# Performance work log

Measured on AMD Instinct MI355X. Metric: run time of the kernel, lower is better.

## Reference

```python
import jax, jax.numpy as jnp
import numpy as np
import math

B, N, IN_DIM, HID, OUT = 16, 1024, 3, 32, 4
RATIO = 0.2
K1 = math.ceil(RATIO * N)    # 205 nodes kept after pool 1
K2 = math.ceil(RATIO * K1)   # 41 nodes kept after pool 2
AVG_DEG = 16.0
BN_EPS = 1e-5


def setup_inputs() -> dict:
    key = jax.random.key(0)
    ks = jax.random.split(key, 16)
    x = jax.random.normal(ks[0], (B, N, IN_DIM), jnp.float32)
    # sparse random undirected adjacency (binary edge weights = 1), no self loops
    u = jax.random.uniform(ks[1], (B, N, N))
    A = (u < (AVG_DEG / N)).astype(jnp.float32)
    A = jnp.maximum(A, jnp.swapaxes(A, -1, -2))
    A = A * (1.0 - jnp.eye(N, dtype=jnp.float32))
    g = lambda i, shp: (jax.random.normal(ks[i], shp, jnp.float32) * 0.1)
    params = dict(
        Wd0=g(2, (IN_DIM, HID)), bd0=jnp.zeros((HID,), jnp.float32),
        Wd1=g(3, (HID, HID)),    bd1=jnp.zeros((HID,), jnp.float32),
        Wd2=g(4, (HID, HID)),    bd2=jnp.zeros((HID,), jnp.float32),
        Wu0=g(5, (HID, HID)),    bu0=jnp.zeros((HID,), jnp.float32),
        Wu1=g(6, (HID, HID)),    bu1=jnp.zeros((HID,), jnp.float32),
        p1=g(7, (HID,)), p2=g(8, (HID,)),
        gamma=jnp.ones((HID,), jnp.float32), beta=jnp.zeros((HID,), jnp.float32),
        W1=g(9, (HID, HID)),  b1=jnp.zeros((HID,), jnp.float32),
        W2=g(10, (HID, HID)), b2=jnp.zeros((HID,), jnp.float32),
        W3=g(11, (HID, OUT)), b3=jnp.zeros((OUT,), jnp.float32),
    )
    return {"x": x, "adj": A, **params}


def _gcn(A, x, W, b):
    # GCNConv(improved=True): A_hat = A + 2I, symmetric normalization
    n = A.shape[-1]
    A_hat = A + 2.0 * jnp.eye(n, dtype=A.dtype)
    deg = A_hat.sum(-1)                              # [B, n]
    dis = jnp.where(deg > 0, jax.lax.rsqrt(deg), 0.0)
    A_norm = dis[..., :, None] * A_hat * dis[..., None, :]
    return jnp.einsum('bij,bjf->bif', A_norm, x @ W) + b


def _augment(A):
    # GraphUNet.augment_adj: add self loops (w=1), square adjacency, drop diag
    n = A.shape[-1]
    eye = jnp.eye(n, dtype=A.dtype)
    Bm = A + eye
    A2 = jnp.einsum('bij,bjk->bik', Bm, Bm)
    return A2 * (1.0 - eye)


def _topk_pool(A, x, p, k):
    # TopKPooling: score = tanh(x.p / ||p||), keep top-k nodes per graph
    score = jnp.tanh((x @ p) / jnp.linalg.norm(p))   # [B, n]
    vals, perm = jax.lax.top_k(score, k)             # descending, matches PyG
    bidx = jnp.arange(x.shape[0])[:, None]
    x_p = x[bidx, perm] * vals[..., None]
    A_p = A[bidx[..., None], perm[:, :, None], perm[:, None, :]]
    return A_p, x_p, perm


def reference(x, adj, Wd0, bd0, Wd1, bd1, Wd2, bd2, Wu0, bu0, Wu1, bu1,
              p1, p2, gamma, beta, W1, b1, W2, b2, W3, b3):
    bidx = jnp.arange(x.shape[0])[:, None]
    # ---- GraphUNet down path ----
    h0 = jax.nn.relu(_gcn(adj, x, Wd0, bd0))
    A1, h, perm1 = _topk_pool(_augment(adj), h0, p1, K1)
    h1 = jax.nn.relu(_gcn(A1, h, Wd1, bd1))
    A2, h, perm2 = _topk_pool(_augment(A1), h1, p2, K2)
    h = jax.nn.relu(_gcn(A2, h, Wd2, bd2))
    # ---- up path (sum_res=True) ----
    up = jnp.zeros_like(h1).at[bidx, perm2].set(h)
    h = jax.nn.relu(_gcn(A1, h1 + up, Wu0, bu0))
    up = jnp.zeros_like(h0).at[bidx, perm1].set(h)
    h = _gcn(adj, h0 + up, Wu1, bu1)   # last up conv: no activation
    # ---- BatchNorm1d over all nodes (training-mode batch stats, biased var) ----
    mean = h.mean((0, 1))
    var = h.var((0, 1))
    hn = (h - mean) * jax.lax.rsqrt(var + BN_EPS) * gamma + beta
    # ---- outnetwork MLP (dropout = identity in eval), LeakyReLU slope 0.01 ----
    r = jax.nn.leaky_relu(hn @ W1 + b1)
    r = jax.nn.leaky_relu(r @ W2 + b2)
    r = r @ W3 + b3
    return r.at[..., 0].set(jax.nn.sigmoid(r[..., 0]))
```

## Files before the change

kernel.cpp:

```cpp
#include <hip/hip_runtime.h>
#include <cmath>

#define BB 16
#define NN 1024
#define KK1 205
#define KK2 42
#define CAP 96

__global__ void k_deg_csr(const float* __restrict__ adj, const float* __restrict__ x,
                          const float* __restrict__ W,
                          float* __restrict__ dis0, int* __restrict__ ncnt,
                          int* __restrict__ nbr, unsigned long long* __restrict__ mask,
                          float* __restrict__ dxw) {
  int row = blockIdx.x * 4 + (threadIdx.x >> 6);
  int lane = threadIdx.x & 63;
  const float* ar = adj + (size_t)row * NN;
  int base = 0;
  for (int c = 0; c < 16; ++c) {
    float v = ar[c * 64 + lane];
    unsigned long long m = __ballot(v != 0.0f);
    if (lane == c) mask[(size_t)row * 16 + c] = m;
    if (v != 0.0f) {
      int pos = base + __popcll(m & ((1ull << lane) - 1ull));
      if (pos < CAP) nbr[(size_t)row * CAP + pos] = c * 64 + lane;
    }
    base += __popcll(m);
  }
  float dis = rsqrtf((float)base + 2.0f);
  if (lane == 0) {
    ncnt[row] = base < CAP ? base : CAP;
    dis0[row] = dis;
  }
  if (lane < 32) {
    float x0 = x[row * 3], x1 = x[row * 3 + 1], x2 = x[row * 3 + 2];
    float s = x0 * W[lane] + x1 * W[32 + lane] + x2 * W[64 + lane];
    dxw[(size_t)row * 32 + lane] = s * dis;
  }
}

template<bool RELU>
__global__ void k_spmm(const float* __restrict__ dxw, const float* __restrict__ dis,
                       const int* __restrict__ ncnt, const int* __restrict__ nbr,
                       const float* __restrict__ bias, float* __restrict__ out) {
  int tid = threadIdx.x;
  int g = tid >> 5, f = tid & 31;
  int node = blockIdx.x * 8 + g;
  int b = node >> 10;
  int cnt = ncnt[node];
  const int* lst = nbr + (size_t)node * CAP;
  const float* dbase = dxw + ((size_t)(b << 10) << 5);
  float a0 = 0.f, a1 = 0.f, a2 = 0.f, a3 = 0.f;
  int k = 0;
  for (; k + 4 <= cnt; k += 4) {
    int4 j4 = *(const int4*)(lst + k);
    a0 += dbase[(size_t)j4.x * 32 + f];
    a1 += dbase[(size_t)j4.y * 32 + f];
    a2 += dbase[(size_t)j4.z * 32 + f];
    a3 += dbase[(size_t)j4.w * 32 + f];
  }
  for (; k < cnt; ++k) a0 += dbase[(size_t)lst[k] * 32 + f];
  float acc = (a0 + a1) + (a2 + a3);
  acc += 2.0f * dxw[(size_t)node * 32 + f];
  float r = dis[node] * acc + bias[f];
  if (RELU) r = fmaxf(r, 0.f);
  out[(size_t)node * 32 + f] = r;
}

template<int MPAD>
__global__ void k_topk(const float* __restrict__ h, const float* __restrict__ p,
                       int M, int K, int* __restrict__ perm, float* __restrict__ vals,
                       int* __restrict__ inv) {
  __shared__ unsigned long long skey[MPAD];
  int b = blockIdx.x, t = threadIdx.x;
  float nn = 0.f;
#pragma unroll
  for (int k = 0; k < 32; ++k) nn += p[k] * p[k];
  unsigned int ordv;
  if (t < M) {
    const float* hr = h + (size_t)(b * M + t) * 32;
    float d = 0.f;
#pragma unroll
    for (int k = 0; k < 32; ++k) d += hr[k] * p[k];
    float v = tanhf(d / sqrtf(nn));
    unsigned int u = __float_as_uint(v);
    if (u == 0x80000000u) u = 0u;
    ordv = (u & 0x80000000u) ? ~u : (u | 0x80000000u);
    inv[b * M + t] = -1;
  } else {
    ordv = 0u;
  }
  skey[t] = ((unsigned long long)(~ordv) << 32) | (unsigned int)t;
  __syncthreads();
  for (int k = 2; k <= MPAD; k <<= 1) {
    for (int j = k >> 1; j > 0; j >>= 1) {
      int ixj = t ^ j;
      if (ixj > t) {
        unsigned long long a = skey[t], c = skey[ixj];
        bool up = ((t & k) == 0);
        if (up == (a > c)) { skey[t] = c; skey[ixj] = a; }
      }
      __syncthreads();
    }
  }
  if (t < K) {
    unsigned long long kk = skey[t];
    unsigned int ord = ~(unsigned int)(kk >> 32);
    unsigned int u = (ord & 0x80000000u) ? (ord & 0x7FFFFFFFu) : ~ord;
    int idx = (int)(kk & 0xFFFFFFFFull);
    perm[b * K + t] = idx;
    vals[b * K + t] = __uint_as_float(u);
    inv[b * M + idx] = t;
  }
}

__global__ void k_buildA1(const unsigned long long* __restrict__ mask,
                          const int* __restrict__ perm1, float* __restrict__ A1,
                          float* __restrict__ dis1) {
  __shared__ unsigned long long smT[16 * KK1];
  __shared__ int sp[KK1];
  int blk = blockIdx.x;
  int b = blk / 52, chunk = blk - b * 52;
  int t = threadIdx.x;
  if (t < KK1) sp[t] = perm1[b * KK1 + t];
  __syncthreads();
  for (int q = t; q < KK1 * 16; q += 256) {
    int i = q >> 4, w = q & 15;
    smT[w * KK1 + i] = mask[((size_t)(b * NN + sp[i])) * 16 + w];
  }
  __syncthreads();
  int wave = t >> 6, lane = t & 63;
  int i = chunk * 4 + wave;
  if (i < KK1) {
    unsigned long long r[16];
#pragma unroll
    for (int w = 0; w < 16; ++w) r[w] = smT[w * KK1 + i];
    float rowsum = 0.f;
    for (int j = lane; j < KK1; j += 64) {
      int cnt = 0;
#pragma unroll
      for (int w = 0; w < 16; ++w) cnt += __popcll(r[w] & smT[w * KK1 + j]);
      int pj = sp[j];
      float edge = (float)((r[pj >> 6] >> (pj & 63)) & 1ull);
      float v = (j == i) ? 0.f : ((float)cnt + 2.f * edge);
      A1[((size_t)(b * KK1) + i) * KK1 + j] = v;
      rowsum += v;
    }
#pragma unroll
    for (int o = 32; o; o >>= 1) rowsum += __shfl_xor(rowsum, o);
    if (lane == 0) dis1[b * KK1 + i] = rsqrtf(rowsum + 2.0f);
  }
}

__global__ void k_xw32g(const float* __restrict__ h, const int* __restrict__ perm,
                        const float* __restrict__ vals, const float* __restrict__ W,
                        const float* __restrict__ dis, int M, int K,
                        float* __restrict__ out) {
  int idx = blockIdx.x * 256 + threadIdx.x;
  int f = idx & 31; int q = idx >> 5;
  int b = q / K;
  int src = perm[q];
  const float* xr = h + (size_t)(b * M + src) * 32;
  float s = 0.f;
#pragma unroll
  for (int k = 0; k < 32; ++k) s += xr[k] * W[k * 32 + f];
  out[idx] = s * dis[q] * vals[q];
}

__global__ void k_xw32u(const float* __restrict__ h, const float* __restrict__ up,
                        const int* __restrict__ inv, const float* __restrict__ W,
                        const float* __restrict__ dis, int M, int K,
                        float* __restrict__ out) {
  int idx = blockIdx.x * 256 + threadIdx.x;
  int f = idx & 31; int node = idx >> 5;
  int b = node / M;
  int iv = inv[node];
  const float* xr = h + (size_t)node * 32;
  float s = 0.f;
  if (iv >= 0) {
    const float* ur = up + (size_t)(b * K + iv) * 32;
#pragma unroll
    for (int k = 0; k < 32; ++k) s += (xr[k] + ur[k]) * W[k * 32 + f];
  } else {
#pragma unroll
    for (int k = 0; k < 32; ++k) s += xr[k] * W[k * 32 + f];
  }
  out[idx] = s * dis[node];
}

template<bool RELU>
__global__ __launch_bounds__(256) void k_dense_apply(
    const float* __restrict__ A, const float* __restrict__ t,
    const float* __restrict__ dis, const float* __restrict__ bias,
    int M, float* __restrict__ out) {
  int row = blockIdx.x;
  int b = row / M, i = row - b * M;
  int tid = threadIdx.x;
  int g = tid >> 5, f = tid & 31;
  const float* Ar = A + (size_t)row * M;
  const float* tb = t + (size_t)b * M * 32;
  float acc = 0.f;
  for (int j = g; j < M; j += 8)
    acc += Ar[j] * tb[j * 32 + f];
  __shared__ float ls[8][32];
  ls[g][f] = acc;
  __syncthreads();
  if (tid < 32) {
    float s = 0.f;
#pragma unroll
    for (int q = 0; q < 8; ++q) s += ls[q][tid];
    s += 2.0f * tb[i * 32 + tid];
    float r = dis[row] * s + bias[tid];
    if (RELU) r = fmaxf(r, 0.f);
    out[(size_t)row * 32 + tid] = r;
  }
}

__global__ void k_buildA2(const float* __restrict__ A1, const int* __restrict__ perm2,
                          float* __restrict__ A2, float* __restrict__ dis2) {
  __shared__ float gsum[8];
  int row = blockIdx.x;
  int b = row / KK2, i = row - b * KK2;
  int g = threadIdx.x >> 5, lane = threadIdx.x & 31;
  int pi = perm2[b * KK2 + i];
  const float* Ri = A1 + ((size_t)(b * KK1 + pi)) * KK1;
  float part = 0.f;
  for (int j = g; j < KK2; j += 8) {
    int pj = perm2[b * KK2 + j];
    const float* Rj = A1 + ((size_t)(b * KK1 + pj)) * KK1;
    float s = 0.f;
    for (int k = lane; k < KK1; k += 32) s += Ri[k] * Rj[k];
#pragma unroll
    for (int o = 16; o; o >>= 1) s += __shfl_xor(s, o, 32);
    float v = (i == j) ? 0.f : (s + 2.0f * Ri[pj]);
    if (lane == 0) {
      A2[((size_t)(b * KK2) + i) * KK2 + j] = v;
      part += v;
    }
  }
  if (lane == 0) gsum[g] = part;
  __syncthreads();
  if (threadIdx.x == 0) {
    float s = 0.f;
#pragma unroll
    for (int q = 0; q < 8; ++q) s += gsum[q];
    dis2[row] = rsqrtf(s + 2.0f);
  }
}

__global__ void k_bnstats(const float* __restrict__ h, float* __restrict__ pacc) {
  int t = threadIdx.x;
  int f = t & 31, g = t >> 5;
  int rowBase = blockIdx.x * 128;
  float s = 0.f, sq = 0.f;
  for (int r = g; r < 128; r += 8) {
    float v = h[(size_t)(rowBase + r) * 32 + f];
    s += v; sq += v * v;
  }
  __shared__ float ls[8][32], lq[8][32];
  ls[g][f] = s; lq[g][f] = sq;
  __syncthreads();
  if (t < 32) {
    float S = 0.f, Q = 0.f;
#pragma unroll
    for (int i = 0; i < 8; ++i) { S += ls[i][t]; Q += lq[i][t]; }
    pacc[blockIdx.x * 64 + t] = S;
    pacc[blockIdx.x * 64 + 32 + t] = Q;
  }
}

__global__ __launch_bounds__(64) void k_mlp(
    const float* __restrict__ h, const float* __restrict__ pacc,
    const float* __restrict__ gamma, const float* __restrict__ beta,
    const float* __restrict__ W1, const float* __restrict__ b1,
    const float* __restrict__ W2, const float* __restrict__ b2,
    const float* __restrict__ W3, const float* __restrict__ b3,
    float* __restrict__ out) {
  __shared__ float sW1[1024], sW2[1024], sW3[128];
  __shared__ float sb1[32], sb2[32], sb3[4], sscale[32], sshift[32];
  int t = threadIdx.x;
  {
    const float4* W1v = (const float4*)W1; float4* d1 = (float4*)sW1;
#pragma unroll
    for (int i = 0; i < 4; ++i) d1[t + i * 64] = W1v[t + i * 64];
    const float4* W2v = (const float4*)W2; float4* d2 = (float4*)sW2;
#pragma unroll
    for (int i = 0; i < 4; ++i) d2[t + i * 64] = W2v[t + i * 64];
    if (t < 32) ((float4*)sW3)[t] = ((const float4*)W3)[t];
    if (t < 32) { sb1[t] = b1[t]; sb2[t] = b2[t]; }
    if (t < 4) sb3[t] = b3[t];
    if (t < 32) {
      float S = 0.f, Q = 0.f;
      for (int q = 0; q < 128; ++q) { S += pacc[q * 64 + t]; Q += pacc[q * 64 + 32 + t]; }
      const float inv = 1.0f / (float)(BB * NN);
      float m = S * inv;
      float v = Q * inv - m * m;
      float sc = gamma[t] * rsqrtf(v + 1e-5f);
      sscale[t] = sc;
      sshift[t] = beta[t] - m * sc;
    }
  }
  __syncthreads();
  int node = blockIdx.x * 64 + t;
  const float4* hr = (const float4*)(h + (size_t)node * 32);
  float hn[32];
#pragma unroll
  for (int i = 0; i < 8; ++i) {
    float4 x = hr[i];
    hn[i * 4 + 0] = x.x * sscale[i * 4 + 0] + sshift[i * 4 + 0];
    hn[i * 4 + 1] = x.y * sscale[i * 4 + 1] + sshift[i * 4 + 1];
    hn[i * 4 + 2] = x.z * sscale[i * 4 + 2] + sshift[i * 4 + 2];
    hn[i * 4 + 3] = x.w * sscale[i * 4 + 3] + sshift[i * 4 + 3];
  }
  float r1[32];
#pragma unroll
  for (int f = 0; f < 32; ++f) r1[f] = sb1[f];
#pragma unroll
  for (int k = 0; k < 32; ++k) {
    float a = hn[k];
#pragma unroll
    for (int f = 0; f < 32; ++f) r1[f] += a * sW1[k * 32 + f];
  }
#pragma unroll
  for (int f = 0; f < 32; ++f) r1[f] = r1[f] > 0.f ? r1[f] : 0.01f * r1[f];
  float r2[32];
#pragma unroll
  for (int f = 0; f < 32; ++f) r2[f] = sb2[f];
#pragma unroll
  for (int k = 0; k < 32; ++k) {
    float a = r1[k];
#pragma unroll
    for (int f = 0; f < 32; ++f) r2[f] += a * sW2[k * 32 + f];
  }
#pragma unroll
  for (int f = 0; f < 32; ++f) r2[f] = r2[f] > 0.f ? r2[f] : 0.01f * r2[f];
  float r3[4];
#pragma unroll
  for (int c = 0; c < 4; ++c) r3[c] = sb3[c];
#pragma unroll
  for (int k = 0; k < 32; ++k) {
    float a = r2[k];
#pragma unroll
    for (int c = 0; c < 4; ++c) r3[c] += a * sW3[k * 4 + c];
  }
  float4 o;
  o.x = 1.0f / (1.0f + expf(-r3[0]));
  o.y = r3[1]; o.z = r3[2]; o.w = r3[3];
  ((float4*)out)[node] = o;
}

extern "C" void kernel_launch(void* const* d_in, const int* in_sizes, int n_in,
                              void* d_out, int out_size, void* d_ws, size_t ws_size,
                              hipStream_t stream) {
  const float* x    = (const float*)d_in[0];
  const float* adj  = (const float*)d_in[1];
  const float* Wd0  = (const float*)d_in[2];
  const float* bd0  = (const float*)d_in[3];
  const float* Wd1  = (const float*)d_in[4];
  const float* bd1  = (const float*)d_in[5];
  const float* Wd2  = (const float*)d_in[6];
  const float* bd2  = (const float*)d_in[7];
  const float* Wu0  = (const float*)d_in[8];
  const float* bu0  = (const float*)d_in[9];
  const float* Wu1  = (const float*)d_in[10];
  const float* bu1  = (const float*)d_in[11];
  const float* p1   = (const float*)d_in[12];
  const float* p2   = (const float*)d_in[13];
  const float* gamma= (const float*)d_in[14];
  const float* beta = (const float*)d_in[15];
  const float* W1   = (const float*)d_in[16];
  const float* b1   = (const float*)d_in[17];
  const float* W2   = (const float*)d_in[18];
  const float* b2   = (const float*)d_in[19];
  const float* W3   = (const float*)d_in[20];
  const float* b3   = (const float*)d_in[21];
  float* out = (float*)d_out;

  char* w = (char*)d_ws;
  auto alloc = [&](size_t bytes) -> void* {
    void* p = (void*)w;
    w += (bytes + 255) & ~(size_t)255;
    return p;
  };
  float* dis0 = (float*)alloc(BB * NN * 4);
  int*   ncnt = (int*)alloc(BB * NN * 4);
  int*   nbr  = (int*)alloc((size_t)BB * NN * CAP * 4);
  unsigned long long* mask = (unsigned long long*)alloc((size_t)BB * NN * 16 * 8);
  float* dxw  = (float*)alloc((size_t)BB * NN * 32 * 4);
  float* h0   = (float*)alloc((size_t)BB * NN * 32 * 4);
  int*   perm1= (int*)alloc(BB * KK1 * 4);
  float* vals1= (float*)alloc(BB * KK1 * 4);
  int*   inv1 = (int*)alloc(BB * NN * 4);
  float* A1   = (float*)alloc((size_t)BB * KK1 * KK1 * 4);
  float* dis1 = (float*)alloc(BB * KK1 * 4);
  float* t1   = (float*)alloc((size_t)BB * KK1 * 32 * 4);
  float* h1   = (float*)alloc((size_t)BB * KK1 * 32 * 4);
  int*   perm2= (int*)alloc(BB * KK2 * 4);
  float* vals2= (float*)alloc(BB * KK2 * 4);
  int*   inv2 = (int*)alloc(BB * KK1 * 4);
  float* A2   = (float*)alloc((size_t)BB * KK2 * KK2 * 4);
  float* dis2 = (float*)alloc(BB * KK2 * 4);
  float* t2   = (float*)alloc((size_t)BB * KK2 * 32 * 4);
  float* h2   = (float*)alloc((size_t)BB * KK2 * 32 * 4);
  float* hu0  = (float*)alloc((size_t)BB * KK1 * 32 * 4);
  float* hfin = (float*)alloc((size_t)BB * NN * 32 * 4);
  float* pacc = (float*)alloc(128 * 64 * 4);

  const int TOT_N32  = BB * NN * 32;
  const int TOT_K132 = BB * KK1 * 32;
  const int TOT_K232 = BB * KK2 * 32;

  k_deg_csr<<<BB * NN / 4, 256, 0, stream>>>(adj, x, Wd0, dis0, ncnt, nbr, mask, dxw);
  k_spmm<true><<<BB * NN / 8, 256, 0, stream>>>(dxw, dis0, ncnt, nbr, bd0, h0);
  k_topk<1024><<<BB, 1024, 0, stream>>>(h0, p1, NN, KK1, perm1, vals1, inv1);
  k_buildA1<<<BB * 52, 256, 0, stream>>>(mask, perm1, A1, dis1);
  k_xw32g<<<TOT_K132 / 256, 256, 0, stream>>>(h0, perm1, vals1, Wd1, dis1, NN, KK1, t1);
  k_dense_apply<true><<<BB * KK1, 256, 0, stream>>>(A1, t1, dis1, bd1, KK1, h1);
  k_topk<256><<<BB, 256, 0, stream>>>(h1, p2, KK1, KK2, perm2, vals2, inv2);
  k_buildA2<<<BB * KK2, 256, 0, stream>>>(A1, perm2, A2, dis2);
  k_xw32g<<<TOT_K232 / 256, 256, 0, stream>>>(h1, perm2, vals2, Wd2, dis2, KK1, KK2, t2);
  k_dense_apply<true><<<BB * KK2, 256, 0, stream>>>(A2, t2, dis2, bd2, KK2, h2);
  k_xw32u<<<TOT_K132 / 256, 256, 0, stream>>>(h1, h2, inv2, Wu0, dis1, KK1, KK2, t1);
  k_dense_apply<true><<<BB * KK1, 256, 0, stream>>>(A1, t1, dis1, bu0, KK1, hu0);
  k_xw32u<<<TOT_N32 / 256, 256, 0, stream>>>(h0, hu0, inv1, Wu1, dis0, NN, KK1, dxw);
  k_spmm<false><<<BB * NN / 8, 256, 0, stream>>>(dxw, dis0, ncnt, nbr, bu1, hfin);
  k_bnstats<<<128, 256, 0, stream>>>(hfin, pacc);
  k_mlp<<<BB * NN / 64, 64, 0, stream>>>(hfin, pacc, gamma, beta,
                                         W1, b1, W2, b2, W3, b3, out);
}
```

Before: 305.8 us.

## Fuse score, gather-matmul and BN statistics into producer kernels

Top-k scores are now computed in the epilogues of the spmm and dense-apply kernels, and top-k only sorts the precomputed scores. The gathered x@W projections are folded into buildA1 and buildA2, and the BatchNorm partial sums move into the final spmm. That removes three launches (two xw32g and bnstats) and re-reads of h. In exchange, k_mlp now reduces 2048 partial rows per block instead of 128, and deg_csr loads all 16 adjacency chunks into registers up front.

```diff
diff --git a/kernel.cpp b/kernel.cpp
--- a/kernel.cpp
+++ b/kernel.cpp
@@ -6,6 +6,7 @@
 #define KK1 205
 #define KK2 42
 #define CAP 96
+#define NPACC 2048
 
 __global__ void k_deg_csr(const float* __restrict__ adj, const float* __restrict__ x,
                           const float* __restrict__ W,
@@ -15,14 +16,18 @@
   int row = blockIdx.x * 4 + (threadIdx.x >> 6);
   int lane = threadIdx.x & 63;
   const float* ar = adj + (size_t)row * NN;
+  float v[16];
+#pragma unroll
+  for (int c = 0; c < 16; ++c) v[c] = ar[c * 64 + lane];
   int base = 0;
+  int* nr = nbr + (size_t)row * CAP;
+#pragma unroll
   for (int c = 0; c < 16; ++c) {
-    float v = ar[c * 64 + lane];
-    unsigned long long m = __ballot(v != 0.0f);
+    unsigned long long m = __ballot(v[c] != 0.0f);
     if (lane == c) mask[(size_t)row * 16 + c] = m;
-    if (v != 0.0f) {
+    if (v[c] != 0.0f) {
       int pos = base + __popcll(m & ((1ull << lane) - 1ull));
-      if (pos < CAP) nbr[(size_t)row * CAP + pos] = c * 64 + lane;
+      if (pos < CAP) nr[pos] = c * 64 + lane;
     }
     base += __popcll(m);
   }
@@ -38,10 +43,12 @@
   }
 }
 
-template<bool RELU>
+template<bool RELU, bool SCORE, bool BNSTATS>
 __global__ void k_spmm(const float* __restrict__ dxw, const float* __restrict__ dis,
                        const int* __restrict__ ncnt, const int* __restrict__ nbr,
-                       const float* __restrict__ bias, float* __restrict__ out) {
+                       const float* __restrict__ bias, float* __restrict__ out,
+                       float* __restrict__ score, const float* __restrict__ p,
+                       float* __restrict__ pacc) {
   int tid = threadIdx.x;
   int g = tid >> 5, f = tid & 31;
   int node = blockIdx.x * 8 + g;
@@ -64,58 +71,78 @@
   float r = dis[node] * acc + bias[f];
   if (RELU) r = fmaxf(r, 0.f);
   out[(size_t)node * 32 + f] = r;
-}
-
-template<int MPAD>
-__global__ void k_topk(const float* __restrict__ h, const float* __restrict__ p,
-                       int M, int K, int* __restrict__ perm, float* __restrict__ vals,
-                       int* __restrict__ inv) {
+  if (SCORE) {
+    float pv = p[f];
+    float d = r * pv, pp = pv * pv;
+#pragma unroll
+    for (int o = 16; o; o >>= 1) { d += __shfl_xor(d, o, 32); pp += __shfl_xor(pp, o, 32); }
+    if (f == 0) score[node] = tanhf(d / sqrtf(pp));
+  }
+  if (BNSTATS) {
+    __shared__ float bs[8][32], bq[8][32];
+    bs[g][f] = r; bq[g][f] = r * r;
+    __syncthreads();
+    if (tid < 32) {
+      float S = 0.f, Q = 0.f;
+#pragma unroll
+      for (int q = 0; q < 8; ++q) { S += bs[q][tid]; Q += bq[q][tid]; }
+      pacc[blockIdx.x * 64 + tid] = S;
+      pacc[blockIdx.x * 64 + 32 + tid] = Q;
+    }
+  }
+}
+
+template<int M, int MPAD, int K, int NT>
+__global__ void k_topk(const float* __restrict__ score, int* __restrict__ perm,
+                       float* __restrict__ vals, int* __restrict__ inv) {
   __shared__ unsigned long long skey[MPAD];
   int b = blockIdx.x, t = threadIdx.x;
-  float nn = 0.f;
-#pragma unroll
-  for (int k = 0; k < 32; ++k) nn += p[k] * p[k];
-  unsigned int ordv;
-  if (t < M) {
-    const float* hr = h + (size_t)(b * M + t) * 32;
-    float d = 0.f;
-#pragma unroll
-    for (int k = 0; k < 32; ++k) d += hr[k] * p[k];
-    float v = tanhf(d / sqrtf(nn));
-    unsigned int u = __float_as_uint(v);
-    if (u == 0x80000000u) u = 0u;
-    ordv = (u & 0x80000000u) ? ~u : (u | 0x80000000u);
-    inv[b * M + t] = -1;
-  } else {
-    ordv = 0u;
-  }
-  skey[t] = ((unsigned long long)(~ordv) << 32) | (unsigned int)t;
+  for (int idx = t; idx < MPAD; idx += NT) {
+    unsigned int ordv;
+    if (idx < M) {
+      float v = score[b * M + idx];
+      unsigned int u = __float_as_uint(v);
+      if (u == 0x80000000u) u = 0u;
+      ordv = (u & 0x80000000u) ? ~u : (u | 0x80000000u);
+      inv[b * M + idx] = -1;
+    } else {
+      ordv = 0u;
+    }
+    skey[idx] = ((unsigned long long)(~ordv) << 32) | (unsigned int)idx;
+  }
   __syncthreads();
   for (int k = 2; k <= MPAD; k <<= 1) {
     for (int j = k >> 1; j > 0; j >>= 1) {
-      int ixj = t ^ j;
-      if (ixj > t) {
-        unsigned long long a = skey[t], c = skey[ixj];
-        bool up = ((t & k) == 0);
-        if (up == (a > c)) { skey[t] = c; skey[ixj] = a; }
+      for (int idx = t; idx < MPAD; idx += NT) {
+        int ixj = idx ^ j;
+        if (ixj > idx) {
+          unsigned long long a = skey[idx], c = skey[ixj];
+          bool up = ((idx & k) == 0);
+          if (up == (a > c)) { skey[idx] = c; skey[ixj] = a; }
+        }
       }
       __syncthreads();
     }
   }
-  if (t < K) {
-    unsigned long long kk = skey[t];
-    unsigned int ord = ~(unsigned int)(kk >> 32);
-    unsigned int u = (ord & 0x80000000u) ? (ord & 0x7FFFFFFFu) : ~ord;
-    int idx = (int)(kk & 0xFFFFFFFFull);
-    perm[b * K + t] = idx;
-    vals[b * K + t] = __uint_as_float(u);
-    inv[b * M + idx] = t;
+  for (int idx = t; idx < MPAD; idx += NT) {
+    if (idx < K) {
+      unsigned long long kk = skey[idx];
+      unsigned int ord = ~(unsigned int)(kk >> 32);
+      unsigned int u = (ord & 0x80000000u) ? (ord & 0x7FFFFFFFu) : ~ord;
+      int src = (int)(kk & 0xFFFFFFFFull);
+      perm[b * K + idx] = src;
+      vals[b * K + idx] = __uint_as_float(u);
+      inv[b * M + src] = idx;
+    }
   }
 }
 
 __global__ void k_buildA1(const unsigned long long* __restrict__ mask,
-                          const int* __restrict__ perm1, float* __restrict__ A1,
-                          float* __restrict__ dis1) {
+                          const int* __restrict__ perm1,
+                          const float* __restrict__ h0, const float* __restrict__ Wd1,
+                          const float* __restrict__ vals1,
+                          float* __restrict__ A1, float* __restrict__ dis1,
+                          float* __restrict__ t1) {
   __shared__ unsigned long long smT[16 * KK1];
   __shared__ int sp[KK1];
   int blk = blockIdx.x;
@@ -147,23 +174,98 @@
     }
 #pragma unroll
     for (int o = 32; o; o >>= 1) rowsum += __shfl_xor(rowsum, o);
-    if (lane == 0) dis1[b * KK1 + i] = rsqrtf(rowsum + 2.0f);
-  }
-}
-
-__global__ void k_xw32g(const float* __restrict__ h, const int* __restrict__ perm,
-                        const float* __restrict__ vals, const float* __restrict__ W,
-                        const float* __restrict__ dis, int M, int K,
-                        float* __restrict__ out) {
-  int idx = blockIdx.x * 256 + threadIdx.x;
-  int f = idx & 31; int q = idx >> 5;
-  int b = q / K;
-  int src = perm[q];
-  const float* xr = h + (size_t)(b * M + src) * 32;
-  float s = 0.f;
-#pragma unroll
-  for (int k = 0; k < 32; ++k) s += xr[k] * W[k * 32 + f];
-  out[idx] = s * dis[q] * vals[q];
+    float dis = rsqrtf(rowsum + 2.0f);
+    if (lane == 0) dis1[b * KK1 + i] = dis;
+    if (lane < 32) {
+      const float* hr = h0 + (size_t)(b * NN + sp[i]) * 32;
+      float s = 0.f;
+#pragma unroll
+      for (int k = 0; k < 32; ++k) s += hr[k] * Wd1[k * 32 + lane];
+      t1[((size_t)(b * KK1) + i) * 32 + lane] = s * dis * vals1[b * KK1 + i];
+    }
+  }
+}
+
+template<bool RELU, bool SCORE>
+__global__ __launch_bounds__(256) void k_dense_apply(
+    const float* __restrict__ A, const float* __restrict__ tbuf,
+    const float* __restrict__ dis, const float* __restrict__ bias,
+    int M, float* __restrict__ out, float* __restrict__ score,
+    const float* __restrict__ p) {
+  int row = blockIdx.x;
+  int b = row / M, i = row - b * M;
+  int tid = threadIdx.x;
+  int g = tid >> 5, f = tid & 31;
+  const float* Ar = A + (size_t)row * M;
+  const float* tb = tbuf + (size_t)b * M * 32;
+  float acc = 0.f;
+  for (int j = g; j < M; j += 8)
+    acc += Ar[j] * tb[j * 32 + f];
+  __shared__ float ls[8][32];
+  ls[g][f] = acc;
+  __syncthreads();
+  if (tid < 32) {
+    float s = 0.f;
+#pragma unroll
+    for (int q = 0; q < 8; ++q) s += ls[q][tid];
+    s += 2.0f * tb[i * 32 + tid];
+    float r = dis[row] * s + bias[tid];
+    if (RELU) r = fmaxf(r, 0.f);
+    out[(size_t)row * 32 + tid] = r;
+    if (SCORE) {
+      float pv = p[tid];
+      float d = r * pv, pp = pv * pv;
+#pragma unroll
+      for (int o = 16; o; o >>= 1) { d += __shfl_xor(d, o, 32); pp += __shfl_xor(pp, o, 32); }
+      if (tid == 0) score[row] = tanhf(d / sqrtf(pp));
+    }
+  }
+}
+
+__global__ void k_buildA2(const float* __restrict__ A1, const int* __restrict__ perm2,
+                          const float* __restrict__ h1, const float* __restrict__ Wd2,
+                          const float* __restrict__ vals2,
+                          float* __restrict__ A2, float* __restrict__ dis2,
+                          float* __restrict__ t2) {
+  __shared__ float gsum[8];
+  __shared__ float ds2s;
+  int row = blockIdx.x;
+  int b = row / KK2, i = row - b * KK2;
+  int g = threadIdx.x >> 5, lane = threadIdx.x & 31;
+  int pi = perm2[b * KK2 + i];
+  const float* Ri = A1 + ((size_t)(b * KK1 + pi)) * KK1;
+  float part = 0.f;
+  for (int j = g; j < KK2; j += 8) {
+    int pj = perm2[b * KK2 + j];
+    const float* Rj = A1 + ((size_t)(b * KK1 + pj)) * KK1;
+    float s = 0.f;
+    for (int k = lane; k < KK1; k += 32) s += Ri[k] * Rj[k];
+#pragma unroll
+    for (int o = 16; o; o >>= 1) s += __shfl_xor(s, o, 32);
+    float v = (i == j) ? 0.f : (s + 2.0f * Ri[pj]);
+    if (lane == 0) {
+      A2[((size_t)(b * KK2) + i) * KK2 + j] = v;
+      part += v;
+    }
+  }
+  if (lane == 0) gsum[g] = part;
+  __syncthreads();
+  if (threadIdx.x == 0) {
+    float s = 0.f;
+#pragma unroll
+    for (int q = 0; q < 8; ++q) s += gsum[q];
+    float d2 = rsqrtf(s + 2.0f);
+    dis2[row] = d2;
+    ds2s = d2;
+  }
+  __syncthreads();
+  if (threadIdx.x < 32) {
+    const float* hr = h1 + (size_t)(b * KK1 + pi) * 32;
+    float s = 0.f;
+#pragma unroll
+    for (int k = 0; k < 32; ++k) s += hr[k] * Wd2[k * 32 + threadIdx.x];
+    t2[(size_t)row * 32 + threadIdx.x] = s * ds2s * vals2[row];
+  }
 }
 
 __global__ void k_xw32u(const float* __restrict__ h, const float* __restrict__ up,
@@ -187,87 +289,6 @@
   out[idx] = s * dis[node];
 }
 
-template<bool RELU>
-__global__ __launch_bounds__(256) void k_dense_apply(
-    const float* __restrict__ A, const float* __restrict__ t,
-    const float* __restrict__ dis, const float* __restrict__ bias,
-    int M, float* __restrict__ out) {
-  int row = blockIdx.x;
-  int b = row / M, i = row - b * M;
-  int tid = threadIdx.x;
-  int g = tid >> 5, f = tid & 31;
-  const float* Ar = A + (size_t)row * M;
-  const float* tb = t + (size_t)b * M * 32;
-  float acc = 0.f;
-  for (int j = g; j < M; j += 8)
-    acc += Ar[j] * tb[j * 32 + f];
-  __shared__ float ls[8][32];
-  ls[g][f] = acc;
-  __syncthreads();
-  if (tid < 32) {
-    float s = 0.f;
-#pragma unroll
-    for (int q = 0; q < 8; ++q) s += ls[q][tid];
-    s += 2.0f * tb[i * 32 + tid];
-    float r = dis[row] * s + bias[tid];
-    if (RELU) r = fmaxf(r, 0.f);
-    out[(size_t)row * 32 + tid] = r;
-  }
-}
-
-__global__ void k_buildA2(const float* __restrict__ A1, const int* __restrict__ perm2,
-                          float* __restrict__ A2, float* __restrict__ dis2) {
-  __shared__ float gsum[8];
-  int row = blockIdx.x;
-  int b = row / KK2, i = row - b * KK2;
-  int g = threadIdx.x >> 5, lane = threadIdx.x & 31;
-  int pi = perm2[b * KK2 + i];
-  const float* Ri = A1 + ((size_t)(b * KK1 + pi)) * KK1;
-  float part = 0.f;
-  for (int j = g; j < KK2; j += 8) {
-    int pj = perm2[b * KK2 + j];
-    const float* Rj = A1 + ((size_t)(b * KK1 + pj)) * KK1;
-    float s = 0.f;
-    for (int k = lane; k < KK1; k += 32) s += Ri[k] * Rj[k];
-#pragma unroll
-    for (int o = 16; o; o >>= 1) s += __shfl_xor(s, o, 32);
-    float v = (i == j) ? 0.f : (s + 2.0f * Ri[pj]);
-    if (lane == 0) {
-      A2[((size_t)(b * KK2) + i) * KK2 + j] = v;
-      part += v;
-    }
-  }
-  if (lane == 0) gsum[g] = part;
-  __syncthreads();
-  if (threadIdx.x == 0) {
-    float s = 0.f;
-#pragma unroll
-    for (int q = 0; q < 8; ++q) s += gsum[q];
-    dis2[row] = rsqrtf(s + 2.0f);
-  }
-}
-
-__global__ void k_bnstats(const float* __restrict__ h, float* __restrict__ pacc) {
-  int t = threadIdx.x;
-  int f = t & 31, g = t >> 5;
-  int rowBase = blockIdx.x * 128;
-  float s = 0.f, sq = 0.f;
-  for (int r = g; r < 128; r += 8) {
-    float v = h[(size_t)(rowBase + r) * 32 + f];
-    s += v; sq += v * v;
-  }
-  __shared__ float ls[8][32], lq[8][32];
-  ls[g][f] = s; lq[g][f] = sq;
-  __syncthreads();
-  if (t < 32) {
-    float S = 0.f, Q = 0.f;
-#pragma unroll
-    for (int i = 0; i < 8; ++i) { S += ls[i][t]; Q += lq[i][t]; }
-    pacc[blockIdx.x * 64 + t] = S;
-    pacc[blockIdx.x * 64 + 32 + t] = Q;
-  }
-}
-
 __global__ __launch_bounds__(64) void k_mlp(
     const float* __restrict__ h, const float* __restrict__ pacc,
     const float* __restrict__ gamma, const float* __restrict__ beta,
@@ -277,6 +298,7 @@
     float* __restrict__ out) {
   __shared__ float sW1[1024], sW2[1024], sW3[128];
   __shared__ float sb1[32], sb2[32], sb3[4], sscale[32], sshift[32];
+  __shared__ float red[64];
   int t = threadIdx.x;
   {
     const float4* W1v = (const float4*)W1; float4* d1 = (float4*)sW1;
@@ -288,16 +310,24 @@
     if (t < 32) ((float4*)sW3)[t] = ((const float4*)W3)[t];
     if (t < 32) { sb1[t] = b1[t]; sb2[t] = b2[t]; }
     if (t < 4) sb3[t] = b3[t];
-    if (t < 32) {
-      float S = 0.f, Q = 0.f;
-      for (int q = 0; q < 128; ++q) { S += pacc[q * 64 + t]; Q += pacc[q * 64 + 32 + t]; }
-      const float inv = 1.0f / (float)(BB * NN);
-      float m = S * inv;
-      float v = Q * inv - m * m;
-      float sc = gamma[t] * rsqrtf(v + 1e-5f);
-      sscale[t] = sc;
-      sshift[t] = beta[t] - m * sc;
-    }
+    float a0 = 0.f, a1 = 0.f, a2 = 0.f, a3 = 0.f,
+          a4 = 0.f, a5 = 0.f, a6 = 0.f, a7 = 0.f;
+    for (int q = 0; q < NPACC; q += 8) {
+      a0 += pacc[(q + 0) * 64 + t]; a1 += pacc[(q + 1) * 64 + t];
+      a2 += pacc[(q + 2) * 64 + t]; a3 += pacc[(q + 3) * 64 + t];
+      a4 += pacc[(q + 4) * 64 + t]; a5 += pacc[(q + 5) * 64 + t];
+      a6 += pacc[(q + 6) * 64 + t]; a7 += pacc[(q + 7) * 64 + t];
+    }
+    red[t] = ((a0 + a1) + (a2 + a3)) + ((a4 + a5) + (a6 + a7));
+  }
+  __syncthreads();
+  if (t < 32) {
+    const float inv = 1.0f / (float)(BB * NN);
+    float m = red[t] * inv;
+    float v = red[32 + t] * inv - m * m;
+    float sc = gamma[t] * rsqrtf(v + 1e-5f);
+    sscale[t] = sc;
+    sshift[t] = beta[t] - m * sc;
   }
   __syncthreads();
   int node = blockIdx.x * 64 + t;
@@ -387,6 +417,7 @@
   unsigned long long* mask = (unsigned long long*)alloc((size_t)BB * NN * 16 * 8);
   float* dxw  = (float*)alloc((size_t)BB * NN * 32 * 4);
   float* h0   = (float*)alloc((size_t)BB * NN * 32 * 4);
+  float* score1 = (float*)alloc(BB * NN * 4);
   int*   perm1= (int*)alloc(BB * KK1 * 4);
   float* vals1= (float*)alloc(BB * KK1 * 4);
   int*   inv1 = (int*)alloc(BB * NN * 4);
@@ -394,6 +425,7 @@
   float* dis1 = (float*)alloc(BB * KK1 * 4);
   float* t1   = (float*)alloc((size_t)BB * KK1 * 32 * 4);
   float* h1   = (float*)alloc((size_t)BB * KK1 * 32 * 4);
+  float* score2 = (float*)alloc(BB * KK1 * 4);
   int*   perm2= (int*)alloc(BB * KK2 * 4);
   float* vals2= (float*)alloc(BB * KK2 * 4);
   int*   inv2 = (int*)alloc(BB * KK1 * 4);
@@ -403,27 +435,28 @@
   float* h2   = (float*)alloc((size_t)BB * KK2 * 32 * 4);
   float* hu0  = (float*)alloc((size_t)BB * KK1 * 32 * 4);
   float* hfin = (float*)alloc((size_t)BB * NN * 32 * 4);
-  float* pacc = (float*)alloc(128 * 64 * 4);
+  float* pacc = (float*)alloc((size_t)NPACC * 64 * 4);
 
   const int TOT_N32  = BB * NN * 32;
   const int TOT_K132 = BB * KK1 * 32;
-  const int TOT_K232 = BB * KK2 * 32;
 
   k_deg_csr<<<BB * NN / 4, 256, 0, stream>>>(adj, x, Wd0, dis0, ncnt, nbr, mask, dxw);
-  k_spmm<true><<<BB * NN / 8, 256, 0, stream>>>(dxw, dis0, ncnt, nbr, bd0, h0);
-  k_topk<1024><<<BB, 1024, 0, stream>>>(h0, p1, NN, KK1, perm1, vals1, inv1);
-  k_buildA1<<<BB * 52, 256, 0, stream>>>(mask, perm1, A1, dis1);
-  k_xw32g<<<TOT_K132 / 256, 256, 0, stream>>>(h0, perm1, vals1, Wd1, dis1, NN, KK1, t1);
-  k_dense_apply<true><<<BB * KK1, 256, 0, stream>>>(A1, t1, dis1, bd1, KK1, h1);
-  k_topk<256><<<BB, 256, 0, stream>>>(h1, p2, KK1, KK2, perm2, vals2, inv2);
-  k_buildA2<<<BB * KK2, 256, 0, stream>>>(A1, perm2, A2, dis2);
-  k_xw32g<<<TOT_K232 / 256, 256, 0, stream>>>(h1, perm2, vals2, Wd2, dis2, KK1, KK2, t2);
-  k_dense_apply<true><<<BB * KK2, 256, 0, stream>>>(A2, t2, dis2, bd2, KK2, h2);
+  k_spmm<true, true, false><<<BB * NN / 8, 256, 0, stream>>>(
+      dxw, dis0, ncnt, nbr, bd0, h0, score1, p1, nullptr);
+  k_topk<NN, 1024, KK1, 1024><<<BB, 1024, 0, stream>>>(score1, perm1, vals1, inv1);
+  k_buildA1<<<BB * 52, 256, 0, stream>>>(mask, perm1, h0, Wd1, vals1, A1, dis1, t1);
+  k_dense_apply<true, true><<<BB * KK1, 256, 0, stream>>>(
+      A1, t1, dis1, bd1, KK1, h1, score2, p2);
+  k_topk<KK1, 256, KK2, 256><<<BB, 256, 0, stream>>>(score2, perm2, vals2, inv2);
+  k_buildA2<<<BB * KK2, 256, 0, stream>>>(A1, perm2, h1, Wd2, vals2, A2, dis2, t2);
+  k_dense_apply<true, false><<<BB * KK2, 256, 0, stream>>>(
+      A2, t2, dis2, bd2, KK2, h2, nullptr, nullptr);
   k_xw32u<<<TOT_K132 / 256, 256, 0, stream>>>(h1, h2, inv2, Wu0, dis1, KK1, KK2, t1);
-  k_dense_apply<true><<<BB * KK1, 256, 0, stream>>>(A1, t1, dis1, bu0, KK1, hu0);
+  k_dense_apply<true, false><<<BB * KK1, 256, 0, stream>>>(
+      A1, t1, dis1, bu0, KK1, hu0, nullptr, nullptr);
   k_xw32u<<<TOT_N32 / 256, 256, 0, stream>>>(h0, hu0, inv1, Wu1, dis0, NN, KK1, dxw);
-  k_spmm<false><<<BB * NN / 8, 256, 0, stream>>>(dxw, dis0, ncnt, nbr, bu1, hfin);
-  k_bnstats<<<128, 256, 0, stream>>>(hfin, pacc);
+  k_spmm<false, false, true><<<BB * NN / 8, 256, 0, stream>>>(
+      dxw, dis0, ncnt, nbr, bu1, hfin, nullptr, nullptr, pacc);
   k_mlp<<<BB * NN / 64, 64, 0, stream>>>(hfin, pacc, gamma, beta,
                                          W1, b1, W2, b2, W3, b3, out);
 }
```

New measurement: 306.1 us. No clear change (+0.1%).
